# Kernel optimization log

Measured on AMD Instinct MI355X. Metric: run time of the kernel, lower is better.

Reference implementation:

```python
import jax, jax.numpy as jnp
import numpy as np

B, N = 8, 64
EMB, CD, NL = 32, 24, 3          # emb_dim, cloud_dim, output degrees l=0,1,2 (cloudord)
NB, H = 3, 100                   # radial basis count, radial hidden width
RADIUS = 2.0                     # neighborradius
CLOUD_OUT = CD * NL**2 + EMB     # 24*9 + 32 = 248 (cloud_res concat)
RES_OUT = 2 * CLOUD_OUT          # 496 (AtomResiduals doubles channels)
FF = 128                         # ffl1size // 1


def spherical_harmonics(u):
    # real SH on unit vectors, se3cnn component order (y,z,x for l=1)
    x, y, z = u[..., 0], u[..., 1], u[..., 2]
    Y0 = jnp.full(x.shape + (1,), 0.28209479177, dtype=u.dtype)
    c1 = 0.48860251190
    Y1 = c1 * jnp.stack([y, z, x], -1)
    c2a, c2b = 1.09254843059, 0.31539156525
    Y2 = jnp.stack([c2a * x * y, c2a * y * z, c2b * (3.0 * z * z - 1.0),
                    c2a * x * z, 0.5 * c2a * (x * x - y * y)], -1)
    return [Y0, Y1, Y2]


def setup_inputs() -> dict:
    key = jax.random.key(0)
    ks = jax.random.split(key, 12)
    g = lambda i, shape, s=0.1: jax.random.normal(ks[i], shape, jnp.float32) * s
    return dict(
        xyz=jax.random.normal(ks[0], (B, N, 3), jnp.float32),
        features=jax.random.randint(ks[1], (B, N), 0, 6),
        emb=g(2, (6, EMB), 1.0),
        rW1=g(3, (NB, H)), rb1=jnp.zeros((H,), jnp.float32),
        rW2=g(4, (H, H)), rb2=jnp.zeros((H,), jnp.float32),
        rW3=g(5, (H, NL * CD * EMB)), rb3=jnp.zeros((NL * CD * EMB,), jnp.float32),
        resW=g(6, (CLOUD_OUT, CLOUD_OUT)), resb=jnp.zeros((CLOUD_OUT,), jnp.float32),
        res_gamma=jnp.ones((CLOUD_OUT,), jnp.float32),
        res_beta=jnp.zeros((CLOUD_OUT,), jnp.float32),
        cW=g(7, (RES_OUT, FF)), cb=jnp.zeros((FF,), jnp.float32),
        c_gamma=jnp.ones((FF,), jnp.float32), c_beta=jnp.zeros((FF,), jnp.float32),
        oW=g(8, (FF, 1)), ob=jnp.zeros((1,), jnp.float32),
    )


def reference(xyz, features, emb, rW1, rb1, rW2, rb2, rW3, rb3,
              resW, resb, res_gamma, res_beta, cW, cb, c_gamma, c_beta, oW, ob):
    eps = 1e-8
    f = emb[features]                                     # [B,N,EMB] scalar (l=0) features
    rij = xyz[:, None, :, :] - xyz[:, :, None, :]         # r_j - r_i  [B,N,N,3]
    d = jnp.sqrt(jnp.sum(rij * rij, -1) + eps)            # [B,N,N]
    mask = ((d < RADIUS) & (~jnp.eye(N, dtype=bool))).astype(f.dtype)
    # CosineBasisModel: cos^2 bumps centered at linspace(0, RADIUS, NB)
    radii = jnp.linspace(0.0, RADIUS, NB)
    step = radii[1] - radii[0]
    u = jnp.abs(d[..., None] - radii) / step
    basis = jnp.where(u < 1.0, jnp.cos(0.5 * jnp.pi * u) ** 2, 0.0)  # [B,N,N,NB]
    sp = lambda x: jax.nn.softplus(5.0 * x) / 5.0          # rescaled Softplus(beta=5)
    h = sp(basis @ rW1 + rb1)
    h = sp(h @ rW2 + rb2)
    R = (h @ rW3 + rb3).reshape(B, N, N, NL, CD, EMB)      # per-pair radial weights
    # contract scalar input channels first (keeps intermediates small): [B,N,N,L,U]
    t = jnp.einsum('bijluv,bjv->bijlu', R, f) / jnp.sqrt(float(EMB))
    Ys = spherical_harmonics(rij / d[..., None])
    inv = (1.0 / jnp.sqrt(jnp.maximum(mask.sum(-1), 1.0)))[:, :, None, None]
    outs = []
    for l, Y in enumerate(Ys):
        o = jnp.einsum('bij,bijm,biju->bium', mask, Y, t[..., l, :])  # [B,N,U,2l+1]
        outs.append((o * inv).reshape(B, N, CD * (2 * l + 1)))
    conv = jnp.concatenate(outs, -1)                       # [B,N,216]
    feats = jnp.concatenate([f, conv], -1)                 # cloud_res concat [B,N,248]
    # AtomResiduals: Linear -> BatchNorm(batch stats) -> relu, concat with input
    x2 = feats.reshape(B * N, CLOUD_OUT) @ resW + resb
    mu, var = x2.mean(0), x2.var(0)
    x2 = jax.nn.relu((x2 - mu) / jnp.sqrt(var + 1e-5) * res_gamma + res_beta)
    feats = jnp.concatenate([feats, x2.reshape(B, N, CLOUD_OUT)], -1)  # [B,N,496]
    pooled = feats.mean(1)                                 # mean collation [B,496]
    h2 = jax.nn.leaky_relu(pooled @ cW + cb, 0.01)
    mu2, var2 = h2.mean(0), h2.var(0)
    h2 = jax.nn.leaky_relu((h2 - mu2) / jnp.sqrt(var2 + 1e-5) * c_gamma + c_beta, 0.01)
    return jax.nn.sigmoid(h2 @ oW + ob)                    # [B,1]
```

## Files before the change

kernel.cpp:

```cpp
#include <hip/hip_runtime.h>
#include <hip/hip_bf16.h>

#define BB   8
#define NN   64
#define EMB  32
#define CD   24
#define HH   100
#define LU   72
#define COUT 248
#define RESO 496
#define FF   128
#define TT   2048

__device__ __forceinline__ float sp5(float x) {
    float z = 5.0f * x;
    float t = __expf(-fabsf(z));
    return 0.2f * (fmaxf(z, 0.0f) + __logf(1.0f + t));
}
__device__ __forceinline__ float4 ld4(const float* p) { return *reinterpret_cast<const float4*>(p); }
__device__ __forceinline__ void st4(float* p, float4 v) { *reinterpret_cast<float4*>(p) = v; }
__device__ __forceinline__ void fma4(float4& a, float s, float4 w) {
    a.x = fmaf(s, w.x, a.x); a.y = fmaf(s, w.y, a.y);
    a.z = fmaf(s, w.z, a.z); a.w = fmaf(s, w.w, a.w);
}

__global__ __launch_bounds__(256) void k0a_w3f(
    const float* __restrict__ rW3, const float* __restrict__ rb3,
    const float* __restrict__ emb, float* __restrict__ W3f_all, float* __restrict__ tb_all)
{
    const int t = blockIdx.x / 10, kc = blockIdx.x % 10;
    __shared__ float embt[EMB];
    if (threadIdx.x < EMB) embt[threadIdx.x] = emb[t * EMB + threadIdx.x];
    __syncthreads();
    for (int idx = threadIdx.x; idx < 10 * LU; idx += 256) {
        const int k = kc * 10 + idx / LU, lu = idx % LU;
        const float* w = rW3 + (size_t)k * (LU * EMB) + lu * EMB;
        float acc = 0.f;
#pragma unroll
        for (int v4 = 0; v4 < EMB / 4; ++v4) {
            float4 wv = ld4(w + 4 * v4);
            acc += wv.x * embt[4 * v4] + wv.y * embt[4 * v4 + 1]
                 + wv.z * embt[4 * v4 + 2] + wv.w * embt[4 * v4 + 3];
        }
        W3f_all[(size_t)t * HH * LU + k * LU + lu] = acc;
    }
    if (kc == 0 && threadIdx.x < LU) {
        const float* w = rb3 + threadIdx.x * EMB;
        float acc = 0.f;
        for (int v = 0; v < EMB; ++v) acc += w[v] * embt[v];
        tb_all[t * LU + threadIdx.x] = acc;
    }
}

__global__ __launch_bounds__(256) void k0b_lut(
    const float* __restrict__ rW1, const float* __restrict__ rb1,
    const float* __restrict__ rW2, const float* __restrict__ rb2,
    const float* __restrict__ W3f_all, const float* __restrict__ tb_all,
    float* __restrict__ LUT)
{
    const int bt = blockIdx.x >> 6, chunk = blockIdx.x & 63;
    const int s0 = chunk * 32;
    const int tid = threadIdx.x;

    __shared__ __align__(16) float h1T[HH * 32];
    __shared__ __align__(16) float h2T[HH * 32];

    {
        const int ik = tid & 31, ug = tid >> 5;
        const float d = (float)(s0 + ik) * (3.0f / 2047.0f);
        float bas[3];
#pragma unroll
        for (int r = 0; r < 3; ++r) {
            float u = fabsf(d - (float)r);
            float c = cosf(1.57079632679489662f * u);
            bas[r] = (u < 1.0f) ? c * c : 0.0f;
        }
#pragma unroll
        for (int uu = 0; uu < 13; ++uu) {
            const int u = ug * 13 + uu;
            if (u < HH) {
                float v = rb1[u] + bas[0] * rW1[u] + bas[1] * rW1[HH + u] + bas[2] * rW1[2 * HH + u];
                h1T[u * 32 + ik] = sp5(v);
            }
        }
    }
    __syncthreads();

    if (tid < 200) {
        const int ut = tid % 25, ig = tid / 25;
        float4 a[4];
        {
            float4 b0 = ld4(&rb2[4 * ut]);
#pragma unroll
            for (int m = 0; m < 4; ++m) a[m] = b0;
        }
#pragma unroll 4
        for (int k = 0; k < HH; ++k) {
            float4 w  = ld4(&rW2[k * HH + 4 * ut]);
            float4 hA = ld4(&h1T[k * 32 + 4 * ig]);
            fma4(a[0], hA.x, w); fma4(a[1], hA.y, w); fma4(a[2], hA.z, w); fma4(a[3], hA.w, w);
        }
#pragma unroll
        for (int m = 0; m < 4; ++m) {
            a[m].x = sp5(a[m].x); a[m].y = sp5(a[m].y); a[m].z = sp5(a[m].z); a[m].w = sp5(a[m].w);
        }
        st4(&h2T[(4 * ut + 0) * 32 + 4 * ig], make_float4(a[0].x, a[1].x, a[2].x, a[3].x));
        st4(&h2T[(4 * ut + 1) * 32 + 4 * ig], make_float4(a[0].y, a[1].y, a[2].y, a[3].y));
        st4(&h2T[(4 * ut + 2) * 32 + 4 * ig], make_float4(a[0].z, a[1].z, a[2].z, a[3].z));
        st4(&h2T[(4 * ut + 3) * 32 + 4 * ig], make_float4(a[0].w, a[1].w, a[2].w, a[3].w));
    }
    __syncthreads();

    if (tid < 144) {
        const int lut = tid % 18, ig = tid / 18;
        const float* W3f = W3f_all + (size_t)bt * HH * LU;
        float4 a[4];
        {
            float4 t0 = ld4(&tb_all[bt * LU + 4 * lut]);
#pragma unroll
            for (int m = 0; m < 4; ++m) a[m] = t0;
        }
#pragma unroll 4
        for (int k = 0; k < HH; ++k) {
            float4 w  = ld4(&W3f[k * LU + 4 * lut]);
            float4 hA = ld4(&h2T[k * 32 + 4 * ig]);
            fma4(a[0], hA.x, w); fma4(a[1], hA.y, w); fma4(a[2], hA.z, w); fma4(a[3], hA.w, w);
        }
        const float s = 0.17677669529663688f;
        float* base = LUT + ((size_t)bt * TT + s0) * LU;
#pragma unroll
        for (int m = 0; m < 4; ++m) {
            const int smp = 4 * ig + m;
            st4(&base[smp * LU + 4 * lut], make_float4(a[m].x * s, a[m].y * s, a[m].z * s, a[m].w * s));
        }
    }
}

__global__ __launch_bounds__(256) void k2_conv(
    const float* __restrict__ xyz, const int* __restrict__ feat,
    const float* __restrict__ emb, const float* __restrict__ LUT,
    const float* __restrict__ resW, const float* __restrict__ resb,
    float* __restrict__ feats, float* __restrict__ x2pre)
{
    const int b = blockIdx.x >> 6, i = blockIdx.x & 63;
    const int tid = threadIdx.x;
    __shared__ __align__(16) float xj[NN * 3];
    __shared__ int   tys[NN];
    __shared__ float dpos[NN];
    __shared__ __align__(16) float mYT[9 * 68];
    __shared__ __align__(16) float tlT[LU * 68];
    __shared__ __align__(16) float fs[COUT];
    __shared__ float inv_s;

    if (tid < 48) st4(&xj[tid * 4], ld4(&xyz[b * NN * 3 + tid * 4]));
    if (tid >= 64 && tid < 128) tys[tid - 64] = feat[b * NN + (tid - 64)];
    if (tid >= 128 && tid < 160) fs[tid - 128] = emb[feat[b * NN + i] * EMB + (tid - 128)];
    __syncthreads();

    if (tid < 64) {
        const int jj = tid;
        float dx = xj[jj * 3 + 0] - xj[i * 3 + 0];
        float dy = xj[jj * 3 + 1] - xj[i * 3 + 1];
        float dz = xj[jj * 3 + 2] - xj[i * 3 + 2];
        float d = sqrtf(dx * dx + dy * dy + dz * dz + 1e-8f);
        float m = (d < 2.0f && jj != i) ? 1.0f : 0.0f;
        float ux = dx / d, uy = dy / d, uz = dz / d;
        mYT[0 * 68 + jj] = m * 0.28209479177f;
        mYT[1 * 68 + jj] = m * 0.48860251190f * uy;
        mYT[2 * 68 + jj] = m * 0.48860251190f * uz;
        mYT[3 * 68 + jj] = m * 0.48860251190f * ux;
        mYT[4 * 68 + jj] = m * 1.09254843059f * ux * uy;
        mYT[5 * 68 + jj] = m * 1.09254843059f * uy * uz;
        mYT[6 * 68 + jj] = m * 0.31539156525f * (3.0f * uz * uz - 1.0f);
        mYT[7 * 68 + jj] = m * 1.09254843059f * ux * uz;
        mYT[8 * 68 + jj] = m * 0.54627421529f * (ux * ux - uy * uy);
        dpos[jj] = fminf(d, 3.0f) * (2047.0f / 3.0f);
        unsigned long long bal = __ballot(m > 0.5f);
        if (jj == 0) inv_s = rsqrtf(fmaxf((float)__popcll(bal), 1.0f));
    }
    __syncthreads();

    for (int idx = tid; idx < NN * LU; idx += 256) {
        const int jj = idx / LU, lu = idx - jj * LU;
        const float pos = dpos[jj];
        int i0 = (int)pos; i0 = (i0 > TT - 2) ? (TT - 2) : i0;
        const float fr = pos - (float)i0;
        const float* rowp = LUT + ((size_t)tys[jj] * TT + i0) * LU + lu;
        const float v0 = rowp[0], v1 = rowp[LU];
        tlT[lu * 68 + jj] = v0 + fr * (v1 - v0);
    }
    __syncthreads();

    if (tid < 216) {
        int l, u, m, yoff;
        if (tid < 24)      { l = 0; u = tid; m = 0; yoff = 0; }
        else if (tid < 96) { int q = tid - 24; l = 1; u = q / 3; m = q % 3; yoff = 1; }
        else               { int q = tid - 96; l = 2; u = q / 5; m = q % 5; yoff = 4; }
        const int lu = l * CD + u, yr = yoff + m;
        float acc = 0.f;
#pragma unroll
        for (int j4 = 0; j4 < 16; ++j4) {
            float4 y = ld4(&mYT[yr * 68 + 4 * j4]);
            float4 t = ld4(&tlT[lu * 68 + 4 * j4]);
            acc += y.x * t.x + y.y * t.y + y.z * t.z + y.w * t.w;
        }
        fs[EMB + tid] = acc * inv_s;
    }
    __syncthreads();

    if (tid < COUT) {
        const size_t row = (size_t)blockIdx.x;
        feats[row * COUT + tid] = fs[tid];
        float acc = resb[tid];
#pragma unroll 4
        for (int k4 = 0; k4 < COUT / 4; ++k4) {
            float4 f4 = ld4(&fs[4 * k4]);
            acc = fmaf(f4.x, resW[(4 * k4 + 0) * COUT + tid], acc);
            acc = fmaf(f4.y, resW[(4 * k4 + 1) * COUT + tid], acc);
            acc = fmaf(f4.z, resW[(4 * k4 + 2) * COUT + tid], acc);
            acc = fmaf(f4.w, resW[(4 * k4 + 3) * COUT + tid], acc);
        }
        x2pre[row * COUT + tid] = acc;
    }
}

__global__ __launch_bounds__(256) void k4_stats(
    const float* __restrict__ x2pre, float* __restrict__ stats)
{
    const int c0 = blockIdx.x * 8;
    const int col = threadIdx.x & 7, r0 = threadIdx.x >> 3;
    float s = 0.f, s2 = 0.f;
#pragma unroll
    for (int p = 0; p < 16; ++p) {
        const int r = r0 + 32 * p;
        const float v = x2pre[(size_t)r * COUT + c0 + col];
        s += v; s2 += v * v;
    }
    __shared__ float rs[256], rq[256];
    rs[threadIdx.x] = s; rq[threadIdx.x] = s2;
    __syncthreads();
    for (int off = 128; off >= 8; off >>= 1) {
        if (threadIdx.x < off) { rs[threadIdx.x] += rs[threadIdx.x + off]; rq[threadIdx.x] += rq[threadIdx.x + off]; }
        __syncthreads();
    }
    if (threadIdx.x < 8) {
        const float mu  = rs[threadIdx.x] * (1.0f / 512.0f);
        const float var = rq[threadIdx.x] * (1.0f / 512.0f) - mu * mu;
        stats[c0 + threadIdx.x]        = mu;
        stats[COUT + c0 + threadIdx.x] = 1.0f / sqrtf(var + 1e-5f);
    }
}

__global__ __launch_bounds__(512) void k5_pool(
    const float* __restrict__ feats, const float* __restrict__ x2pre,
    const float* __restrict__ stats,
    const float* __restrict__ gamma, const float* __restrict__ beta,
    float* __restrict__ pp)
{
    const int b = blockIdx.x >> 3, seg = blockIdx.x & 7;
    const int c = threadIdx.x;
    if (c >= RESO) return;
    float acc = 0.f;
    if (c < COUT) {
#pragma unroll
        for (int ii = 0; ii < 8; ++ii)
            acc += feats[(size_t)(b * NN + seg * 8 + ii) * COUT + c];
    } else {
        const int cc = c - COUT;
        const float mu = stats[cc], rstd = stats[COUT + cc];
        const float g = gamma[cc], be = beta[cc];
#pragma unroll
        for (int ii = 0; ii < 8; ++ii) {
            const float v = (x2pre[(size_t)(b * NN + seg * 8 + ii) * COUT + cc] - mu) * rstd * g + be;
            acc += fmaxf(v, 0.f);
        }
    }
    pp[(seg * BB + b) * RESO + c] = acc * (1.0f / (float)NN);
}

__global__ __launch_bounds__(1024) void k6_head(
    const float* __restrict__ pp,
    const float* __restrict__ cW, const float* __restrict__ cb,
    const float* __restrict__ c_gamma, const float* __restrict__ c_beta,
    const float* __restrict__ oW, const float* __restrict__ ob,
    float* __restrict__ out)
{
    const int tid = threadIdx.x;
    const int o = tid & 127, chunk = tid >> 7;
    __shared__ __align__(16) float psT[RESO * BB];
    __shared__ __align__(16) float part[8 * 8 * FF];
    __shared__ __align__(16) float red[FF * BB];
    for (int idx = tid; idx < RESO * BB; idx += 1024) {
        const int bb = idx / RESO, k = idx - bb * RESO;
        float s = 0.f;
#pragma unroll
        for (int seg = 0; seg < 8; ++seg) s += pp[seg * (BB * RESO) + idx];
        psT[k * BB + bb] = s;
    }
    __syncthreads();

    float4 aA = make_float4(0.f, 0.f, 0.f, 0.f), aB = aA;
    const int kbase = chunk * 62;
#pragma unroll 2
    for (int kk = 0; kk < 62; ++kk) {
        const int k = kbase + kk;
        const float w = cW[k * FF + o];
        fma4(aA, w, ld4(&psT[k * BB]));
        fma4(aB, w, ld4(&psT[k * BB + 4]));
    }
    part[0 * 1024 + chunk * FF + o] = aA.x;
    part[1 * 1024 + chunk * FF + o] = aA.y;
    part[2 * 1024 + chunk * FF + o] = aA.z;
    part[3 * 1024 + chunk * FF + o] = aA.w;
    part[4 * 1024 + chunk * FF + o] = aB.x;
    part[5 * 1024 + chunk * FF + o] = aB.y;
    part[6 * 1024 + chunk * FF + o] = aB.z;
    part[7 * 1024 + chunk * FF + o] = aB.w;
    __syncthreads();

    if (tid < FF) {
        float h[8];
#pragma unroll
        for (int q = 0; q < 8; ++q) {
            float s = 0.f;
#pragma unroll
            for (int ch = 0; ch < 8; ++ch) s += part[q * 1024 + ch * FF + tid];
            h[q] = s + cb[tid];
        }
        float mu = 0.f;
#pragma unroll
        for (int q = 0; q < 8; ++q) { h[q] = (h[q] >= 0.f) ? h[q] : 0.01f * h[q]; mu += h[q]; }
        mu *= 0.125f;
        float var = 0.f;
#pragma unroll
        for (int q = 0; q < 8; ++q) { float dd = h[q] - mu; var += dd * dd; }
        var *= 0.125f;
        const float rstd = 1.0f / sqrtf(var + 1e-5f);
        const float g = c_gamma[tid], be = c_beta[tid], wo = oW[tid];
#pragma unroll
        for (int q = 0; q < 8; ++q) {
            float v = (h[q] - mu) * rstd * g + be;
            h[q] = ((v >= 0.f) ? v : 0.01f * v) * wo;
        }
        st4(&red[tid * 8],     make_float4(h[0], h[1], h[2], h[3]));
        st4(&red[tid * 8 + 4], make_float4(h[4], h[5], h[6], h[7]));
    }
    __syncthreads();
    for (int off = 64; off >= 1; off >>= 1) {
        if (tid < off) {
            float4 x0 = ld4(&red[tid * 8]),     y0 = ld4(&red[(tid + off) * 8]);
            float4 x1 = ld4(&red[tid * 8 + 4]), y1 = ld4(&red[(tid + off) * 8 + 4]);
            st4(&red[tid * 8],     make_float4(x0.x + y0.x, x0.y + y0.y, x0.z + y0.z, x0.w + y0.w));
            st4(&red[tid * 8 + 4], make_float4(x1.x + y1.x, x1.y + y1.y, x1.z + y1.z, x1.w + y1.w));
        }
        __syncthreads();
    }
    if (tid < BB) out[tid] = 1.0f / (1.0f + __expf(-(red[tid] + ob[0])));
}

extern "C" void kernel_launch(void* const* d_in, const int* in_sizes, int n_in,
                              void* d_out, int out_size, void* d_ws, size_t ws_size,
                              hipStream_t stream)
{
    const float* xyz  = (const float*)d_in[0];
    const int*   feat = (const int*)  d_in[1];
    const float* emb  = (const float*)d_in[2];
    const float* rW1  = (const float*)d_in[3];
    const float* rb1  = (const float*)d_in[4];
    const float* rW2  = (const float*)d_in[5];
    const float* rb2  = (const float*)d_in[6];
    const float* rW3  = (const float*)d_in[7];
    const float* rb3  = (const float*)d_in[8];
    const float* resW = (const float*)d_in[9];
    const float* resb = (const float*)d_in[10];
    const float* res_gamma = (const float*)d_in[11];
    const float* res_beta  = (const float*)d_in[12];
    const float* cW   = (const float*)d_in[13];
    const float* cb   = (const float*)d_in[14];
    const float* c_gamma = (const float*)d_in[15];
    const float* c_beta  = (const float*)d_in[16];
    const float* oW   = (const float*)d_in[17];
    const float* ob   = (const float*)d_in[18];
    float* out = (float*)d_out;

    char* ws = (char*)d_ws;
    float* LUT     = (float*)ws;
    float* W3f_all = (float*)(ws + 3538944);
    float* tb_all  = (float*)(ws + 3711744);
    float* feats   = (float*)(ws + 3713472);
    float* x2pre   = (float*)(ws + 4221376);
    float* stats   = (float*)(ws + 4729280);
    float* pp      = (float*)(ws + 4731264);

    k0a_w3f <<<60, 256, 0, stream>>>(rW3, rb3, emb, W3f_all, tb_all);
    k0b_lut <<<384, 256, 0, stream>>>(rW1, rb1, rW2, rb2, W3f_all, tb_all, LUT);
    k2_conv <<<BB * NN, 256, 0, stream>>>(xyz, feat, emb, LUT, resW, resb, feats, x2pre);
    k4_stats<<<31, 256, 0, stream>>>(x2pre, stats);
    k5_pool <<<BB * 8, 512, 0, stream>>>(feats, x2pre, stats, res_gamma, res_beta, pp);
    k6_head <<<1, 1024, 0, stream>>>(pp, cW, cb, c_gamma, c_beta, oW, ob, out);
}
```

Baseline: 156.6 us.

## Halve radial LUT to cover only the cutoff and fuse BN/pool/head tail into one kernel

```diff
diff --git a/kernel.cpp b/kernel.cpp
--- a/kernel.cpp
+++ b/kernel.cpp
@@ -10,7 +10,7 @@
 #define COUT 248
 #define RESO 496
 #define FF   128
-#define TT   2048
+#define TT   1024
 
 __device__ __forceinline__ float sp5(float x) {
     float z = 5.0f * x;
@@ -58,7 +58,7 @@
     const float* __restrict__ W3f_all, const float* __restrict__ tb_all,
     float* __restrict__ LUT)
 {
-    const int bt = blockIdx.x >> 6, chunk = blockIdx.x & 63;
+    const int bt = blockIdx.x >> 5, chunk = blockIdx.x & 31;
     const int s0 = chunk * 32;
     const int tid = threadIdx.x;
 
@@ -67,7 +67,7 @@
 
     {
         const int ik = tid & 31, ug = tid >> 5;
-        const float d = (float)(s0 + ik) * (3.0f / 2047.0f);
+        const float d = (float)(s0 + ik) * (2.0f / 1023.0f);
         float bas[3];
 #pragma unroll
         for (int r = 0; r < 3; ++r) {
@@ -174,7 +174,7 @@
         mYT[6 * 68 + jj] = m * 0.31539156525f * (3.0f * uz * uz - 1.0f);
         mYT[7 * 68 + jj] = m * 1.09254843059f * ux * uz;
         mYT[8 * 68 + jj] = m * 0.54627421529f * (ux * ux - uy * uy);
-        dpos[jj] = fminf(d, 3.0f) * (2047.0f / 3.0f);
+        dpos[jj] = fminf(d, 2.0f) * ((float)(TT - 1) * 0.5f);
         unsigned long long bal = __ballot(m > 0.5f);
         if (jj == 0) inv_s = rsqrtf(fmaxf((float)__popcll(bal), 1.0f));
     }
@@ -224,98 +224,95 @@
     }
 }
 
-__global__ __launch_bounds__(256) void k4_stats(
-    const float* __restrict__ x2pre, float* __restrict__ stats)
-{
-    const int c0 = blockIdx.x * 8;
-    const int col = threadIdx.x & 7, r0 = threadIdx.x >> 3;
-    float s = 0.f, s2 = 0.f;
-#pragma unroll
-    for (int p = 0; p < 16; ++p) {
-        const int r = r0 + 32 * p;
-        const float v = x2pre[(size_t)r * COUT + c0 + col];
-        s += v; s2 += v * v;
-    }
-    __shared__ float rs[256], rq[256];
-    rs[threadIdx.x] = s; rq[threadIdx.x] = s2;
-    __syncthreads();
-    for (int off = 128; off >= 8; off >>= 1) {
-        if (threadIdx.x < off) { rs[threadIdx.x] += rs[threadIdx.x + off]; rq[threadIdx.x] += rq[threadIdx.x + off]; }
-        __syncthreads();
-    }
-    if (threadIdx.x < 8) {
-        const float mu  = rs[threadIdx.x] * (1.0f / 512.0f);
-        const float var = rq[threadIdx.x] * (1.0f / 512.0f) - mu * mu;
-        stats[c0 + threadIdx.x]        = mu;
-        stats[COUT + c0 + threadIdx.x] = 1.0f / sqrtf(var + 1e-5f);
-    }
-}
-
-__global__ __launch_bounds__(512) void k5_pool(
+__global__ __launch_bounds__(1024) void kd_tail(
     const float* __restrict__ feats, const float* __restrict__ x2pre,
-    const float* __restrict__ stats,
     const float* __restrict__ gamma, const float* __restrict__ beta,
-    float* __restrict__ pp)
-{
-    const int b = blockIdx.x >> 3, seg = blockIdx.x & 7;
-    const int c = threadIdx.x;
-    if (c >= RESO) return;
-    float acc = 0.f;
-    if (c < COUT) {
-#pragma unroll
-        for (int ii = 0; ii < 8; ++ii)
-            acc += feats[(size_t)(b * NN + seg * 8 + ii) * COUT + c];
-    } else {
-        const int cc = c - COUT;
-        const float mu = stats[cc], rstd = stats[COUT + cc];
-        const float g = gamma[cc], be = beta[cc];
-#pragma unroll
-        for (int ii = 0; ii < 8; ++ii) {
-            const float v = (x2pre[(size_t)(b * NN + seg * 8 + ii) * COUT + cc] - mu) * rstd * g + be;
-            acc += fmaxf(v, 0.f);
-        }
-    }
-    pp[(seg * BB + b) * RESO + c] = acc * (1.0f / (float)NN);
-}
-
-__global__ __launch_bounds__(1024) void k6_head(
-    const float* __restrict__ pp,
     const float* __restrict__ cW, const float* __restrict__ cb,
     const float* __restrict__ c_gamma, const float* __restrict__ c_beta,
     const float* __restrict__ oW, const float* __restrict__ ob,
     float* __restrict__ out)
 {
     const int tid = threadIdx.x;
-    const int o = tid & 127, chunk = tid >> 7;
     __shared__ __align__(16) float psT[RESO * BB];
-    __shared__ __align__(16) float part[8 * 8 * FF];
+    __shared__ __align__(16) float part[8 * 1024];
+    __shared__ __align__(16) float musd[2 * COUT];
     __shared__ __align__(16) float red[FF * BB];
-    for (int idx = tid; idx < RESO * BB; idx += 1024) {
-        const int bb = idx / RESO, k = idx - bb * RESO;
-        float s = 0.f;
-#pragma unroll
-        for (int seg = 0; seg < 8; ++seg) s += pp[seg * (BB * RESO) + idx];
-        psT[k * BB + bb] = s;
-    }
-    __syncthreads();
-
-    float4 aA = make_float4(0.f, 0.f, 0.f, 0.f), aB = aA;
-    const int kbase = chunk * 62;
+
+    {
+        const int q = tid >> 8, cs = tid & 255;
+        float s = 0.f, s2 = 0.f;
+        if (cs < COUT) {
+            const float* p = x2pre + (size_t)(q * 128) * COUT + cs;
+#pragma unroll 4
+            for (int r = 0; r < 128; ++r) { const float v = p[(size_t)r * COUT]; s += v; s2 += v * v; }
+        }
+        part[q * 256 + cs] = s;
+        part[1024 + q * 256 + cs] = s2;
+    }
+    __syncthreads();
+    if (tid < COUT) {
+        const float s  = part[tid] + part[256 + tid] + part[512 + tid] + part[768 + tid];
+        const float s2 = part[1024 + tid] + part[1280 + tid] + part[1536 + tid] + part[1792 + tid];
+        const float mu = s * (1.0f / 512.0f);
+        const float var = s2 * (1.0f / 512.0f) - mu * mu;
+        musd[tid] = mu;
+        musd[COUT + tid] = 1.0f / sqrtf(var + 1e-5f);
+    }
+    __syncthreads();
+
+    {
+        const int b = tid >> 7, cs = tid & 127;
+        const int c1 = cs + 128;
+        const bool f1 = (c1 < COUT);
+        const int cc1 = c1 - COUT;
+        const int cc2 = cs + 8;
+        const int cc3 = cs + 136;
+        const bool v3 = (cc3 < COUT);
+        float mu1 = 0, rs1 = 0, g1 = 0, be1 = 0;
+        if (!f1) { mu1 = musd[cc1]; rs1 = musd[COUT + cc1]; g1 = gamma[cc1]; be1 = beta[cc1]; }
+        const float mu2 = musd[cc2], rs2 = musd[COUT + cc2], g2 = gamma[cc2], be2 = beta[cc2];
+        float mu3 = 0, rs3 = 0, g3 = 0, be3 = 0;
+        if (v3) { mu3 = musd[cc3]; rs3 = musd[COUT + cc3]; g3 = gamma[cc3]; be3 = beta[cc3]; }
+        float a0 = 0.f, a1 = 0.f, a2 = 0.f, a3 = 0.f;
+        const float* fr = feats + (size_t)(b * NN) * COUT;
+        const float* xr = x2pre + (size_t)(b * NN) * COUT;
+        for (int i = 0; i < NN; ++i) {
+            const float* frow = fr + (size_t)i * COUT;
+            const float* xrow = xr + (size_t)i * COUT;
+            a0 += frow[cs];
+            if (f1) a1 += frow[c1];
+            else { const float v = (xrow[cc1] - mu1) * rs1 * g1 + be1; a1 += fmaxf(v, 0.f); }
+            { const float v = (xrow[cc2] - mu2) * rs2 * g2 + be2; a2 += fmaxf(v, 0.f); }
+            if (v3) { const float v = (xrow[cc3] - mu3) * rs3 * g3 + be3; a3 += fmaxf(v, 0.f); }
+        }
+        const float inv = 1.0f / (float)NN;
+        psT[cs * BB + b] = a0 * inv;
+        psT[c1 * BB + b] = a1 * inv;
+        psT[(cs + 256) * BB + b] = a2 * inv;
+        if (v3) psT[(cs + 384) * BB + b] = a3 * inv;
+    }
+    __syncthreads();
+
+    {
+        const int o = tid & 127, chunk = tid >> 7;
+        float4 aA = make_float4(0.f, 0.f, 0.f, 0.f), aB = aA;
+        const int kbase = chunk * 62;
 #pragma unroll 2
-    for (int kk = 0; kk < 62; ++kk) {
-        const int k = kbase + kk;
-        const float w = cW[k * FF + o];
-        fma4(aA, w, ld4(&psT[k * BB]));
-        fma4(aB, w, ld4(&psT[k * BB + 4]));
-    }
-    part[0 * 1024 + chunk * FF + o] = aA.x;
-    part[1 * 1024 + chunk * FF + o] = aA.y;
-    part[2 * 1024 + chunk * FF + o] = aA.z;
-    part[3 * 1024 + chunk * FF + o] = aA.w;
-    part[4 * 1024 + chunk * FF + o] = aB.x;
-    part[5 * 1024 + chunk * FF + o] = aB.y;
-    part[6 * 1024 + chunk * FF + o] = aB.z;
-    part[7 * 1024 + chunk * FF + o] = aB.w;
+        for (int kk = 0; kk < 62; ++kk) {
+            const int k = kbase + kk;
+            const float w = cW[k * FF + o];
+            fma4(aA, w, ld4(&psT[k * BB]));
+            fma4(aB, w, ld4(&psT[k * BB + 4]));
+        }
+        part[0 * 1024 + chunk * FF + o] = aA.x;
+        part[1 * 1024 + chunk * FF + o] = aA.y;
+        part[2 * 1024 + chunk * FF + o] = aA.z;
+        part[3 * 1024 + chunk * FF + o] = aA.w;
+        part[4 * 1024 + chunk * FF + o] = aB.x;
+        part[5 * 1024 + chunk * FF + o] = aB.y;
+        part[6 * 1024 + chunk * FF + o] = aB.z;
+        part[7 * 1024 + chunk * FF + o] = aB.w;
+    }
     __syncthreads();
 
     if (tid < FF) {
@@ -333,7 +330,7 @@
         mu *= 0.125f;
         float var = 0.f;
 #pragma unroll
-        for (int q = 0; q < 8; ++q) { float dd = h[q] - mu; var += dd * dd; }
+        for (int q = 0; q < 8; ++q) { const float dd = h[q] - mu; var += dd * dd; }
         var *= 0.125f;
         const float rstd = 1.0f / sqrtf(var + 1e-5f);
         const float g = c_gamma[tid], be = c_beta[tid], wo = oW[tid];
@@ -385,17 +382,14 @@
 
     char* ws = (char*)d_ws;
     float* LUT     = (float*)ws;
-    float* W3f_all = (float*)(ws + 3538944);
-    float* tb_all  = (float*)(ws + 3711744);
-    float* feats   = (float*)(ws + 3713472);
-    float* x2pre   = (float*)(ws + 4221376);
-    float* stats   = (float*)(ws + 4729280);
-    float* pp      = (float*)(ws + 4731264);
+    float* W3f_all = (float*)(ws + 1769472);
+    float* tb_all  = (float*)(ws + 1942272);
+    float* feats   = (float*)(ws + 1944000);
+    float* x2pre   = (float*)(ws + 2451904);
 
     k0a_w3f <<<60, 256, 0, stream>>>(rW3, rb3, emb, W3f_all, tb_all);
-    k0b_lut <<<384, 256, 0, stream>>>(rW1, rb1, rW2, rb2, W3f_all, tb_all, LUT);
+    k0b_lut <<<192, 256, 0, stream>>>(rW1, rb1, rW2, rb2, W3f_all, tb_all, LUT);
     k2_conv <<<BB * NN, 256, 0, stream>>>(xyz, feat, emb, LUT, resW, resb, feats, x2pre);
-    k4_stats<<<31, 256, 0, stream>>>(x2pre, stats);
-    k5_pool <<<BB * 8, 512, 0, stream>>>(feats, x2pre, stats, res_gamma, res_beta, pp);
-    k6_head <<<1, 1024, 0, stream>>>(pp, cW, cb, c_gamma, c_beta, oW, ob, out);
-}
+    kd_tail <<<1, 1024, 0, stream>>>(feats, x2pre, res_gamma, res_beta,
+                                     cW, cb, c_gamma, c_beta, oW, ob, out);
+}
```

Measured after the change: 197.2 us. +26.0%, slower.

## Fuse W3 folding into LUT kernel and shrink LUT range to cutoff radius

Applied to the files above, without the earlier changes.

```diff
diff --git a/kernel.cpp b/kernel.cpp
--- a/kernel.cpp
+++ b/kernel.cpp
@@ -10,7 +10,7 @@
 #define COUT 248
 #define RESO 496
 #define FF   128
-#define TT   2048
+#define TT   1024
 
 __device__ __forceinline__ float sp5(float x) {
     float z = 5.0f * x;
@@ -24,16 +24,27 @@
     a.z = fmaf(s, w.z, a.z); a.w = fmaf(s, w.w, a.w);
 }
 
-__global__ __launch_bounds__(256) void k0a_w3f(
+__global__ __launch_bounds__(256) void ka_lut(
+    const float* __restrict__ rW1, const float* __restrict__ rb1,
+    const float* __restrict__ rW2, const float* __restrict__ rb2,
     const float* __restrict__ rW3, const float* __restrict__ rb3,
-    const float* __restrict__ emb, float* __restrict__ W3f_all, float* __restrict__ tb_all)
-{
-    const int t = blockIdx.x / 10, kc = blockIdx.x % 10;
-    __shared__ float embt[EMB];
-    if (threadIdx.x < EMB) embt[threadIdx.x] = emb[t * EMB + threadIdx.x];
-    __syncthreads();
-    for (int idx = threadIdx.x; idx < 10 * LU; idx += 256) {
-        const int k = kc * 10 + idx / LU, lu = idx % LU;
+    const float* __restrict__ emb, float* __restrict__ LUT)
+{
+    const int bt = blockIdx.x >> 5, chunk = blockIdx.x & 31;
+    const int s0 = chunk * 32;
+    const int tid = threadIdx.x;
+
+    __shared__ __align__(16) float embt[EMB];
+    __shared__ __align__(16) float W3fs[HH * LU];
+    __shared__ __align__(16) float tbs[LU];
+    __shared__ __align__(16) float h1T[HH * 32];
+    __shared__ __align__(16) float h2T[HH * 32];
+
+    if (tid < EMB) embt[tid] = emb[bt * EMB + tid];
+    __syncthreads();
+
+    for (int idx = tid; idx < HH * LU; idx += 256) {
+        const int k = idx / LU, lu = idx - k * LU;
         const float* w = rW3 + (size_t)k * (LU * EMB) + lu * EMB;
         float acc = 0.f;
 #pragma unroll
@@ -42,32 +53,19 @@
             acc += wv.x * embt[4 * v4] + wv.y * embt[4 * v4 + 1]
                  + wv.z * embt[4 * v4 + 2] + wv.w * embt[4 * v4 + 3];
         }
-        W3f_all[(size_t)t * HH * LU + k * LU + lu] = acc;
-    }
-    if (kc == 0 && threadIdx.x < LU) {
-        const float* w = rb3 + threadIdx.x * EMB;
+        W3fs[idx] = acc;
+    }
+    if (tid < LU) {
+        const float* w = rb3 + tid * EMB;
         float acc = 0.f;
+#pragma unroll
         for (int v = 0; v < EMB; ++v) acc += w[v] * embt[v];
-        tb_all[t * LU + threadIdx.x] = acc;
-    }
-}
-
-__global__ __launch_bounds__(256) void k0b_lut(
-    const float* __restrict__ rW1, const float* __restrict__ rb1,
-    const float* __restrict__ rW2, const float* __restrict__ rb2,
-    const float* __restrict__ W3f_all, const float* __restrict__ tb_all,
-    float* __restrict__ LUT)
-{
-    const int bt = blockIdx.x >> 6, chunk = blockIdx.x & 63;
-    const int s0 = chunk * 32;
-    const int tid = threadIdx.x;
-
-    __shared__ __align__(16) float h1T[HH * 32];
-    __shared__ __align__(16) float h2T[HH * 32];
+        tbs[tid] = acc;
+    }
 
     {
         const int ik = tid & 31, ug = tid >> 5;
-        const float d = (float)(s0 + ik) * (3.0f / 2047.0f);
+        const float d = (float)(s0 + ik) * (2.0f / 1023.0f);
         float bas[3];
 #pragma unroll
         for (int r = 0; r < 3; ++r) {
@@ -113,16 +111,15 @@
 
     if (tid < 144) {
         const int lut = tid % 18, ig = tid / 18;
-        const float* W3f = W3f_all + (size_t)bt * HH * LU;
         float4 a[4];
         {
-            float4 t0 = ld4(&tb_all[bt * LU + 4 * lut]);
+            float4 t0 = ld4(&tbs[4 * lut]);
 #pragma unroll
             for (int m = 0; m < 4; ++m) a[m] = t0;
         }
 #pragma unroll 4
         for (int k = 0; k < HH; ++k) {
-            float4 w  = ld4(&W3f[k * LU + 4 * lut]);
+            float4 w  = ld4(&W3fs[k * LU + 4 * lut]);
             float4 hA = ld4(&h2T[k * 32 + 4 * ig]);
             fma4(a[0], hA.x, w); fma4(a[1], hA.y, w); fma4(a[2], hA.z, w); fma4(a[3], hA.w, w);
         }
@@ -174,7 +171,7 @@
         mYT[6 * 68 + jj] = m * 0.31539156525f * (3.0f * uz * uz - 1.0f);
         mYT[7 * 68 + jj] = m * 1.09254843059f * ux * uz;
         mYT[8 * 68 + jj] = m * 0.54627421529f * (ux * ux - uy * uy);
-        dpos[jj] = fminf(d, 3.0f) * (2047.0f / 3.0f);
+        dpos[jj] = fminf(d, 2.0f) * ((float)(TT - 1) * 0.5f);
         unsigned long long bal = __ballot(m > 0.5f);
         if (jj == 0) inv_s = rsqrtf(fmaxf((float)__popcll(bal), 1.0f));
     }
@@ -333,7 +330,7 @@
         mu *= 0.125f;
         float var = 0.f;
 #pragma unroll
-        for (int q = 0; q < 8; ++q) { float dd = h[q] - mu; var += dd * dd; }
+        for (int q = 0; q < 8; ++q) { const float dd = h[q] - mu; var += dd * dd; }
         var *= 0.125f;
         const float rstd = 1.0f / sqrtf(var + 1e-5f);
         const float g = c_gamma[tid], be = c_beta[tid], wo = oW[tid];
@@ -384,16 +381,13 @@
     float* out = (float*)d_out;
 
     char* ws = (char*)d_ws;
-    float* LUT     = (float*)ws;
-    float* W3f_all = (float*)(ws + 3538944);
-    float* tb_all  = (float*)(ws + 3711744);
-    float* feats   = (float*)(ws + 3713472);
-    float* x2pre   = (float*)(ws + 4221376);
-    float* stats   = (float*)(ws + 4729280);
-    float* pp      = (float*)(ws + 4731264);
-
-    k0a_w3f <<<60, 256, 0, stream>>>(rW3, rb3, emb, W3f_all, tb_all);
-    k0b_lut <<<384, 256, 0, stream>>>(rW1, rb1, rW2, rb2, W3f_all, tb_all, LUT);
+    float* LUT   = (float*)ws;
+    float* feats = (float*)(ws + 1769472);
+    float* x2pre = (float*)(ws + 2277376);
+    float* stats = (float*)(ws + 2785280);
+    float* pp    = (float*)(ws + 2787264);
+
+    ka_lut  <<<192, 256, 0, stream>>>(rW1, rb1, rW2, rb2, rW3, rb3, emb, LUT);
     k2_conv <<<BB * NN, 256, 0, stream>>>(xyz, feat, emb, LUT, resW, resb, feats, x2pre);
     k4_stats<<<31, 256, 0, stream>>>(x2pre, stats);
     k5_pool <<<BB * 8, 512, 0, stream>>>(feats, x2pre, stats, res_gamma, res_beta, pp);
```

New measurement: 170.9 us. +9.1%, slower.
